# Kernel tuning notes

Measured on AMD Instinct MI355X. Metric: run time of the kernel, lower is better.

## Reference

```python
import jax, jax.numpy as jnp
import numpy as np

DECAY = 0.8
EPS = 1e-05


def setup_inputs() -> dict:
    key = jax.random.key(0)
    k1, k2, k3 = jax.random.split(key, 3)
    B, N, D, H, K = 8, 2048, 64, 1, 8192
    x = jax.random.normal(k1, (B, N, D), dtype=jnp.float32)
    embeddings = jax.random.normal(k2, (H, K, D), dtype=jnp.float32)
    cluster_size = jnp.ones((H, K), dtype=jnp.float32)
    embed_avg = jax.random.normal(k3, (H, K, D), dtype=jnp.float32)
    return {"x": x, "embeddings": embeddings,
            "cluster_size": cluster_size, "embed_avg": embed_avg}


def reference(x, embeddings, cluster_size, embed_avg):
    # x: [B, N, D]; ndim < 4 -> prepend codebook dim h=1, pack to [h, B*N, D]
    B, N, D = x.shape
    H, K, _ = embeddings.shape
    flatten = x.reshape(1, B * N, D)  # h = 1

    # dist = -cdist(flatten, embeddings); argmax(-d) == argmin(d2)
    # squared Euclidean distance via expansion (avoid sqrt; monotone for argmin)
    f2 = jnp.sum(flatten * flatten, axis=-1, keepdims=True)        # [h, n, 1]
    e2 = jnp.sum(embeddings * embeddings, axis=-1)[:, None, :]     # [h, 1, K]
    cross = jnp.einsum('hnd,hkd->hnk', flatten, embeddings)        # [h, n, K]
    d2 = f2 - 2.0 * cross + e2                                     # [h, n, K]
    embed_ind = jnp.argmin(d2, axis=-1)                            # [h, n] int

    # quantize: gather selected codes (== onehot @ embeddings)
    quantize = jnp.take(embeddings[0], embed_ind[0], axis=0).reshape(B, N, D)

    # EMA codebook update (training path) via segment sums (== onehot einsum)
    idx = embed_ind[0]                                             # [B*N]
    cs = jax.ops.segment_sum(jnp.ones_like(idx, dtype=flatten.dtype),
                             idx, num_segments=K)[None, :]         # [h, K]
    embed_sum = jax.ops.segment_sum(flatten[0], idx,
                                    num_segments=K)[None]          # [h, K, D]

    new_cluster_size = cluster_size * DECAY + cs * (1.0 - DECAY)
    new_embed_avg = embed_avg * DECAY + embed_sum * (1.0 - DECAY)

    # laplace smoothing then normalize embed_avg
    total = jnp.sum(new_cluster_size, axis=-1, keepdims=True)      # [h, 1]
    smoothed = (new_cluster_size + EPS) / (total + K * EPS) * total
    embed_normalized = new_embed_avg / smoothed[..., None]         # [h, K, D]

    return quantize, embed_ind.reshape(B, N), embed_normalized, new_cluster_size, new_embed_avg
```

## Files before the change

kernel.cpp:

```cpp
#include <hip/hip_runtime.h>

#define D 64
#define BM 128
#define NCHUNK 8
#define NLIST (2 * NCHUNK)
#define DECAYF 0.8f
#define OMDF 0.2f
#define EPSF 1e-5f
#define INVS 4.8828125e-4f

typedef _Float16 f16;
typedef _Float16 f16x8 __attribute__((ext_vector_type(8)));
typedef float f32x4 __attribute__((ext_vector_type(4)));

__global__ __launch_bounds__(512) void prep_kernel(
    const float* __restrict__ emb, const float* __restrict__ cluster_size,
    f16* __restrict__ eh2, f16* __restrict__ el2, float* __restrict__ e2,
    float* __restrict__ cs_sum, float* __restrict__ ncs, float* __restrict__ nea,
    int K)
{
    __shared__ float red[512];
    int t = blockIdx.x * 512 + threadIdx.x;
    int lane = t & 63;
    int sub  = (t >> 6) & 7;
    int tile = t >> 9;
    int wn = sub >> 2, nf = (sub >> 1) & 1, ks = sub & 1;
    int lrow = lane & 15, lkg = lane >> 4;
    int k  = tile * 64 + wn * 32 + nf * 16 + lrow;
    int d0 = ks * 32 + lkg * 8;

    {
        float4 z = {0.f, 0.f, 0.f, 0.f};
        float4* nea4 = reinterpret_cast<float4*>(nea);
        nea4[t]         = z;
        nea4[t + 65536] = z;
        if (t < 2048) reinterpret_cast<float4*>(ncs)[t] = z;
    }

    const float4* p = reinterpret_cast<const float4*>(emb + (size_t)k * D + d0);
    float4 a = p[0], b = p[1];
    float v[8] = {a.x, a.y, a.z, a.w, b.x, b.y, b.z, b.w};
    union { f16 h[8]; uint4 u; } H, L;
    float part = 0.f;
#pragma unroll
    for (int j = 0; j < 8; ++j) {
        part = fmaf(v[j], v[j], part);
        f16 h = (f16)v[j];
        H.h[j] = h;
        L.h[j] = (f16)((v[j] - (float)h) * 2048.0f);
    }
    reinterpret_cast<uint4*>(eh2)[t] = H.u;
    reinterpret_cast<uint4*>(el2)[t] = L.u;

    red[threadIdx.x] = part;

    if (blockIdx.x < (K >> 9)) {
        float cv = cluster_size[t];
#pragma unroll
        for (int m = 1; m < 64; m <<= 1) cv += __shfl_xor(cv, m, 64);
        if ((threadIdx.x & 63) == 0) atomicAdd(cs_sum, cv);
    }
    __syncthreads();

    if (threadIdx.x < 64) {
        int r = threadIdx.x;
        int rwn = r >> 5, rnf = (r >> 4) & 1, rlr = r & 15;
        float s = 0.f;
#pragma unroll
        for (int kks = 0; kks < 2; ++kks)
#pragma unroll
            for (int g = 0; g < 4; ++g)
                s += red[((rwn * 2 + rnf) * 2 + kks) * 64 + g * 16 + rlr];
        e2[tile * 64 + r] = s;
    }
}

__global__ __launch_bounds__(256, 2) void argmin_kernel(
    const float* __restrict__ x, const f16* __restrict__ eh2, const f16* __restrict__ el2,
    const float* __restrict__ e2, int* __restrict__ pidx, int n, int K)
{
    __shared__ float se2a[1024];

    const int tx   = threadIdx.x;
    const int lane = tx & 63;
    const int wid  = tx >> 6;
    const int wm   = wid >> 1, wn = wid & 1;
    const int lrow = lane & 15;
    const int lkg  = lane >> 4;

    const int chunk = blockIdx.x % NCHUNK;
    const int mblk  = blockIdx.x / NCHUNK;
    const int q0    = mblk * BM;
    const int kc    = K / NCHUNK;
    const int k0    = chunk * kc;
    const int gt0   = chunk * (kc / 64);
    const int NT    = kc / 64;

    f16x8 ah[4][2], al[4][2];
    f32x4 hf2[4];
#pragma unroll
    for (int m = 0; m < 4; ++m) {
        float f2part = 0.f;
#pragma unroll
        for (int ks = 0; ks < 2; ++ks) {
            int row = q0 + wm * 64 + m * 16 + lrow;
            const float4* p = reinterpret_cast<const float4*>(
                x + (size_t)row * D + ks * 32 + lkg * 8);
            float4 va = p[0], vb = p[1];
            float t[8] = {va.x, va.y, va.z, va.w, vb.x, vb.y, vb.z, vb.w};
#pragma unroll
            for (int j = 0; j < 8; ++j) {
                f2part = fmaf(t[j], t[j], f2part);
                float nt = -t[j];
                f16 h = (f16)nt;
                ah[m][ks][j] = h;
                al[m][ks][j] = (f16)((nt - (float)h) * 2048.0f);
            }
        }
        f2part += __shfl_xor(f2part, 16, 64);
        f2part += __shfl_xor(f2part, 32, 64);
#pragma unroll
        for (int r = 0; r < 4; ++r)
            hf2[m][r] = 0.5f * __shfl(f2part, lkg * 4 + r, 64);
    }

    for (int i = tx; i < kc; i += 256) se2a[i] = 0.5f * e2[k0 + i];
    __syncthreads();

    unsigned int pbest[16];
#pragma unroll
    for (int s = 0; s < 16; ++s) pbest[s] = 0xFFFFFFFFu;

    auto LOADB = [&](f16x8 (&BH)[2][2], f16x8 (&BL)[2][2], int ttv) {
        const f16* bhb = eh2 + ((size_t)(gt0 + ttv) << 12);
        const f16* blb = el2 + ((size_t)(gt0 + ttv) << 12);
#pragma unroll
        for (int nf = 0; nf < 2; ++nf)
#pragma unroll
            for (int ks = 0; ks < 2; ++ks) {
                int sub = (wn * 2 + nf) * 2 + ks;
                BH[nf][ks] = *reinterpret_cast<const f16x8*>(bhb + sub * 512 + lane * 8);
                BL[nf][ks] = *reinterpret_cast<const f16x8*>(blb + sub * 512 + lane * 8);
            }
    };

    auto COMPUTE = [&](const f16x8 (&BH)[2][2], const f16x8 (&BL)[2][2], int ttv) {
        const float he0 = se2a[ttv * 64 + wn * 32 + lrow];
        const float he1 = se2a[ttv * 64 + wn * 32 + 16 + lrow];
        const unsigned int tagA = (unsigned int)(ttv * 2);
        const unsigned int tagB = tagA + 1u;
#pragma unroll
        for (int m = 0; m < 4; ++m) {
            f32x4 hh0 = hf2[m] + he0;
            f32x4 hh1 = hf2[m] + he1;
            f32x4 md0 = {0.f, 0.f, 0.f, 0.f};
            f32x4 md1 = {0.f, 0.f, 0.f, 0.f};
            __builtin_amdgcn_s_setprio(1);
            hh0 = __builtin_amdgcn_mfma_f32_16x16x32_f16(ah[m][0], BH[0][0], hh0, 0, 0, 0);
            hh1 = __builtin_amdgcn_mfma_f32_16x16x32_f16(ah[m][0], BH[1][0], hh1, 0, 0, 0);
            hh0 = __builtin_amdgcn_mfma_f32_16x16x32_f16(ah[m][1], BH[0][1], hh0, 0, 0, 0);
            hh1 = __builtin_amdgcn_mfma_f32_16x16x32_f16(ah[m][1], BH[1][1], hh1, 0, 0, 0);
            md0 = __builtin_amdgcn_mfma_f32_16x16x32_f16(al[m][0], BH[0][0], md0, 0, 0, 0);
            md1 = __builtin_amdgcn_mfma_f32_16x16x32_f16(al[m][0], BH[1][0], md1, 0, 0, 0);
            md0 = __builtin_amdgcn_mfma_f32_16x16x32_f16(al[m][1], BH[0][1], md0, 0, 0, 0);
            md1 = __builtin_amdgcn_mfma_f32_16x16x32_f16(al[m][1], BH[1][1], md1, 0, 0, 0);
            md0 = __builtin_amdgcn_mfma_f32_16x16x32_f16(ah[m][0], BL[0][0], md0, 0, 0, 0);
            md1 = __builtin_amdgcn_mfma_f32_16x16x32_f16(ah[m][0], BL[1][0], md1, 0, 0, 0);
            md0 = __builtin_amdgcn_mfma_f32_16x16x32_f16(ah[m][1], BL[0][1], md0, 0, 0, 0);
            md1 = __builtin_amdgcn_mfma_f32_16x16x32_f16(ah[m][1], BL[1][1], md1, 0, 0, 0);
            __builtin_amdgcn_s_setprio(0);
#pragma unroll
            for (int r = 0; r < 4; ++r) {
                float tA = fmaf(md0[r], INVS, hh0[r]);
                float tB = fmaf(md1[r], INVS, hh1[r]);
                unsigned int uA = (__float_as_uint(tA) & 0xFFFFFFE0u) | tagA;
                unsigned int uB = (__float_as_uint(tB) & 0xFFFFFFE0u) | tagB;
                unsigned int w = uA < uB ? uA : uB;
                int s = m * 4 + r;
                pbest[s] = pbest[s] < w ? pbest[s] : w;
            }
        }
    };

    f16x8 bh[2][2], bl[2][2], nh[2][2], nl[2][2];
    LOADB(bh, bl, 0);
#pragma unroll 1
    for (int tt = 0; tt < NT; tt += 2) {
        LOADB(nh, nl, tt + 1);
        COMPUTE(bh, bl, tt);
        if (tt + 2 < NT) LOADB(bh, bl, tt + 2);
        COMPUTE(nh, nl, tt + 1);
    }

#pragma unroll
    for (int s = 0; s < 16; ++s) {
        unsigned int u = pbest[s];
        unsigned int tag = u & 31u;
        int cid = (int)((tag >> 1) << 6) | (int)((tag & 1u) << 4) | (wn << 5) | lrow;
#pragma unroll
        for (int xm = 1; xm < 16; xm <<= 1) {
            unsigned int ou = __shfl_xor(u, xm, 64);
            int          oc = __shfl_xor(cid, xm, 64);
            if (ou < u || (ou == u && oc < cid)) { u = ou; cid = oc; }
        }
        if (lrow == 0) {
            int m = s >> 2, r = s & 3;
            int row = q0 + wm * 64 + m * 16 + lkg * 4 + r;
            pidx[(size_t)(chunk * 2 + wn) * n + row] = k0 + cid;
        }
    }
}

__global__ __launch_bounds__(256) void rerank_kernel(
    const float* __restrict__ x, const float* __restrict__ emb, const float* __restrict__ e2,
    const int* __restrict__ pidx, float* __restrict__ out_ind, float* __restrict__ quant,
    float* __restrict__ embed_sum, float* __restrict__ counts, int n)
{
    int gid  = blockIdx.x * blockDim.x + threadIdx.x;
    int q    = gid >> 6;
    int lane = gid & 63;
    int c    = lane >> 2;
    int j    = lane & 3;
    if (q >= n) return;

    int k = pidx[(size_t)c * n + q];
    const float4* ep = reinterpret_cast<const float4*>(emb + (size_t)k * D);
    const float4* xp = reinterpret_cast<const float4*>(x + (size_t)q * D);

    float a0 = 0.f, a1 = 0.f, a2 = 0.f, a3 = 0.f;
#pragma unroll
    for (int i = 0; i < 4; ++i) {
        float4 e4 = ep[j + 4 * i];
        float4 x4 = xp[j + 4 * i];
        a0 = fmaf(x4.x, e4.x, a0);
        a1 = fmaf(x4.y, e4.y, a1);
        a2 = fmaf(x4.z, e4.z, a2);
        a3 = fmaf(x4.w, e4.w, a3);
    }
    float p = (a0 + a1) + (a2 + a3);
    p += __shfl_xor(p, 1, 64);
    p += __shfl_xor(p, 2, 64);
    float dist = fmaf(p, -2.0f, e2[k]);
    int   bk   = k;

#pragma unroll
    for (int xm = 4; xm < 64; xm <<= 1) {
        float od = __shfl_xor(dist, xm, 64);
        int   ok = __shfl_xor(bk, xm, 64);
        if (od < dist || (od == dist && ok < bk)) { dist = od; bk = ok; }
    }

    float xv = x[(size_t)q * D + lane];
    quant[(size_t)q * D + lane] = emb[(size_t)bk * D + lane];
    atomicAdd(embed_sum + (size_t)bk * D + lane, xv);
    if (lane == 0) {
        out_ind[q] = (float)bk;
        atomicAdd(counts + bk, 1.0f);
    }
}

__global__ __launch_bounds__(256) void ema_kernel(
    const float* __restrict__ cluster_size, const float* __restrict__ embed_avg,
    const float* __restrict__ cs_sum, float* __restrict__ ncs,
    float* __restrict__ nea, float* __restrict__ enorm, int K, int n)
{
    int gid = blockIdx.x * blockDim.x + threadIdx.x;
    if (gid >= K * D) return;
    int k = gid >> 6;
    float total = DECAYF * cs_sum[0] + OMDF * (float)n;
    float cnew  = cluster_size[k] * DECAYF + ncs[k] * OMDF;
    if ((gid & 63) == 0) ncs[k] = cnew;
    float v = embed_avg[gid] * DECAYF + nea[gid] * OMDF;
    nea[gid] = v;
    float smoothed = (cnew + EPSF) / (total + (float)K * EPSF) * total;
    enorm[gid] = v / smoothed;
}

extern "C" void kernel_launch(void* const* d_in, const int* in_sizes, int n_in,
                              void* d_out, int out_size, void* d_ws, size_t ws_size,
                              hipStream_t stream) {
    const float* x            = (const float*)d_in[0];
    const float* emb          = (const float*)d_in[1];
    const float* cluster_size = (const float*)d_in[2];
    const float* embed_avg    = (const float*)d_in[3];

    const int n = in_sizes[0] / D;
    const int K = in_sizes[1] / D;

    float* out     = (float*)d_out;
    float* quant   = out;
    float* out_ind = quant + (size_t)n * D;
    float* enorm   = out_ind + n;
    float* ncs     = enorm + (size_t)K * D;
    float* nea     = ncs + K;

    f16* eh2 = reinterpret_cast<f16*>(enorm);
    f16* el2 = eh2 + (size_t)K * D;

    float* e2     = (float*)d_ws;
    int*   pidx   = (int*)(e2 + K);
    float* cs_sum = (float*)(pidx + (size_t)NLIST * n);

    hipMemsetAsync(cs_sum, 0, sizeof(float), stream);

    prep_kernel<<<K * 8 / 512, 512, 0, stream>>>(
        emb, cluster_size, eh2, el2, e2, cs_sum, ncs, nea, K);
    argmin_kernel<<<(n / BM) * NCHUNK, 256, 0, stream>>>(x, eh2, el2, e2, pidx, n, K);
    rerank_kernel<<<(n * 64 + 255) / 256, 256, 0, stream>>>(
        x, emb, e2, pidx, out_ind, quant, nea, ncs, n);
    ema_kernel<<<(K * D + 255) / 256, 256, 0, stream>>>(
        cluster_size, embed_avg, cs_sum, ncs, nea, enorm, K, n);
}
```

Before: 88.87 us.

## Drop split-fp16 correction MFMAs; keep top-2 candidates per list and rerank more

The argmin pass now uses a single fp16 product instead of the hi/lo split that needed three times the MFMAs and a second codebook copy. To make up for the lost precision, each wave keeps the two best candidates per row instead of one. That doubles the candidate lists, and the exact fp32 rerank kernel then checks 32 candidates per query with 2 lanes each. This cuts matrix-core work and codebook loads, at the cost of more compare logic, more candidate writes and a risk of a wrong argmin when the true best falls outside the fp16 top-2.

Result: slower. 99.14 us (+11.6%).

```diff
diff --git a/kernel.cpp b/kernel.cpp
--- a/kernel.cpp
+++ b/kernel.cpp
@@ -3,11 +3,10 @@
 #define D 64
 #define BM 128
 #define NCHUNK 8
-#define NLIST (2 * NCHUNK)
+#define NLIST (4 * NCHUNK)
 #define DECAYF 0.8f
 #define OMDF 0.2f
 #define EPSF 1e-5f
-#define INVS 4.8828125e-4f
 
 typedef _Float16 f16;
 typedef _Float16 f16x8 __attribute__((ext_vector_type(8)));
@@ -15,7 +14,7 @@
 
 __global__ __launch_bounds__(512) void prep_kernel(
     const float* __restrict__ emb, const float* __restrict__ cluster_size,
-    f16* __restrict__ eh2, f16* __restrict__ el2, float* __restrict__ e2,
+    f16* __restrict__ eh2, float* __restrict__ e2,
     float* __restrict__ cs_sum, float* __restrict__ ncs, float* __restrict__ nea,
     int K)
 {
@@ -40,17 +39,14 @@
     const float4* p = reinterpret_cast<const float4*>(emb + (size_t)k * D + d0);
     float4 a = p[0], b = p[1];
     float v[8] = {a.x, a.y, a.z, a.w, b.x, b.y, b.z, b.w};
-    union { f16 h[8]; uint4 u; } H, L;
+    union { f16 h[8]; uint4 u; } H;
     float part = 0.f;
 #pragma unroll
     for (int j = 0; j < 8; ++j) {
         part = fmaf(v[j], v[j], part);
-        f16 h = (f16)v[j];
-        H.h[j] = h;
-        L.h[j] = (f16)((v[j] - (float)h) * 2048.0f);
+        H.h[j] = (f16)v[j];
     }
     reinterpret_cast<uint4*>(eh2)[t] = H.u;
-    reinterpret_cast<uint4*>(el2)[t] = L.u;
 
     red[threadIdx.x] = part;
 
@@ -76,7 +72,7 @@
 }
 
 __global__ __launch_bounds__(256, 2) void argmin_kernel(
-    const float* __restrict__ x, const f16* __restrict__ eh2, const f16* __restrict__ el2,
+    const float* __restrict__ x, const f16* __restrict__ eh2,
     const float* __restrict__ e2, int* __restrict__ pidx, int n, int K)
 {
     __shared__ float se2a[1024];
@@ -96,7 +92,7 @@
     const int gt0   = chunk * (kc / 64);
     const int NT    = kc / 64;
 
-    f16x8 ah[4][2], al[4][2];
+    f16x8 ah[4][2];
     f32x4 hf2[4];
 #pragma unroll
     for (int m = 0; m < 4; ++m) {
@@ -111,10 +107,7 @@
 #pragma unroll
             for (int j = 0; j < 8; ++j) {
                 f2part = fmaf(t[j], t[j], f2part);
-                float nt = -t[j];
-                f16 h = (f16)nt;
-                ah[m][ks][j] = h;
-                al[m][ks][j] = (f16)((nt - (float)h) * 2048.0f);
+                ah[m][ks][j] = (f16)(-t[j]);
             }
         }
         f2part += __shfl_xor(f2part, 16, 64);
@@ -127,24 +120,22 @@
     for (int i = tx; i < kc; i += 256) se2a[i] = 0.5f * e2[k0 + i];
     __syncthreads();
 
-    unsigned int pbest[16];
-#pragma unroll
-    for (int s = 0; s < 16; ++s) pbest[s] = 0xFFFFFFFFu;
-
-    auto LOADB = [&](f16x8 (&BH)[2][2], f16x8 (&BL)[2][2], int ttv) {
+    unsigned int p1[16], p2[16];
+#pragma unroll
+    for (int s = 0; s < 16; ++s) { p1[s] = 0xFFFFFFFFu; p2[s] = 0xFFFFFFFFu; }
+
+    auto LOADB = [&](f16x8 (&BH)[2][2], int ttv) {
         const f16* bhb = eh2 + ((size_t)(gt0 + ttv) << 12);
-        const f16* blb = el2 + ((size_t)(gt0 + ttv) << 12);
 #pragma unroll
         for (int nf = 0; nf < 2; ++nf)
 #pragma unroll
             for (int ks = 0; ks < 2; ++ks) {
                 int sub = (wn * 2 + nf) * 2 + ks;
                 BH[nf][ks] = *reinterpret_cast<const f16x8*>(bhb + sub * 512 + lane * 8);
-                BL[nf][ks] = *reinterpret_cast<const f16x8*>(blb + sub * 512 + lane * 8);
             }
     };
 
-    auto COMPUTE = [&](const f16x8 (&BH)[2][2], const f16x8 (&BL)[2][2], int ttv) {
+    auto COMPUTE = [&](const f16x8 (&BH)[2][2], int ttv) {
         const float he0 = se2a[ttv * 64 + wn * 32 + lrow];
         const float he1 = se2a[ttv * 64 + wn * 32 + 16 + lrow];
         const unsigned int tagA = (unsigned int)(ttv * 2);
@@ -153,60 +144,65 @@
         for (int m = 0; m < 4; ++m) {
             f32x4 hh0 = hf2[m] + he0;
             f32x4 hh1 = hf2[m] + he1;
-            f32x4 md0 = {0.f, 0.f, 0.f, 0.f};
-            f32x4 md1 = {0.f, 0.f, 0.f, 0.f};
             __builtin_amdgcn_s_setprio(1);
             hh0 = __builtin_amdgcn_mfma_f32_16x16x32_f16(ah[m][0], BH[0][0], hh0, 0, 0, 0);
             hh1 = __builtin_amdgcn_mfma_f32_16x16x32_f16(ah[m][0], BH[1][0], hh1, 0, 0, 0);
             hh0 = __builtin_amdgcn_mfma_f32_16x16x32_f16(ah[m][1], BH[0][1], hh0, 0, 0, 0);
             hh1 = __builtin_amdgcn_mfma_f32_16x16x32_f16(ah[m][1], BH[1][1], hh1, 0, 0, 0);
-            md0 = __builtin_amdgcn_mfma_f32_16x16x32_f16(al[m][0], BH[0][0], md0, 0, 0, 0);
-            md1 = __builtin_amdgcn_mfma_f32_16x16x32_f16(al[m][0], BH[1][0], md1, 0, 0, 0);
-            md0 = __builtin_amdgcn_mfma_f32_16x16x32_f16(al[m][1], BH[0][1], md0, 0, 0, 0);
-            md1 = __builtin_amdgcn_mfma_f32_16x16x32_f16(al[m][1], BH[1][1], md1, 0, 0, 0);
-            md0 = __builtin_amdgcn_mfma_f32_16x16x32_f16(ah[m][0], BL[0][0], md0, 0, 0, 0);
-            md1 = __builtin_amdgcn_mfma_f32_16x16x32_f16(ah[m][0], BL[1][0], md1, 0, 0, 0);
-            md0 = __builtin_amdgcn_mfma_f32_16x16x32_f16(ah[m][1], BL[0][1], md0, 0, 0, 0);
-            md1 = __builtin_amdgcn_mfma_f32_16x16x32_f16(ah[m][1], BL[1][1], md1, 0, 0, 0);
             __builtin_amdgcn_s_setprio(0);
 #pragma unroll
             for (int r = 0; r < 4; ++r) {
-                float tA = fmaf(md0[r], INVS, hh0[r]);
-                float tB = fmaf(md1[r], INVS, hh1[r]);
-                unsigned int uA = (__float_as_uint(tA) & 0xFFFFFFE0u) | tagA;
-                unsigned int uB = (__float_as_uint(tB) & 0xFFFFFFE0u) | tagB;
-                unsigned int w = uA < uB ? uA : uB;
+                unsigned int uA = (__float_as_uint(hh0[r]) & 0xFFFFFFE0u) | tagA;
+                unsigned int uB = (__float_as_uint(hh1[r]) & 0xFFFFFFE0u) | tagB;
+                unsigned int lo = uA < uB ? uA : uB;
+                unsigned int hi = uA < uB ? uB : uA;
                 int s = m * 4 + r;
-                pbest[s] = pbest[s] < w ? pbest[s] : w;
+                unsigned int t1 = p1[s], t2 = p2[s];
+                unsigned int mx = t1 > lo ? t1 : lo;
+                unsigned int mn2 = t2 < hi ? t2 : hi;
+                p1[s] = t1 < lo ? t1 : lo;
+                p2[s] = mx < mn2 ? mx : mn2;
             }
         }
     };
 
-    f16x8 bh[2][2], bl[2][2], nh[2][2], nl[2][2];
-    LOADB(bh, bl, 0);
+    f16x8 bh[2][2], nh[2][2];
+    LOADB(bh, 0);
 #pragma unroll 1
     for (int tt = 0; tt < NT; tt += 2) {
-        LOADB(nh, nl, tt + 1);
-        COMPUTE(bh, bl, tt);
-        if (tt + 2 < NT) LOADB(bh, bl, tt + 2);
-        COMPUTE(nh, nl, tt + 1);
+        LOADB(nh, tt + 1);
+        COMPUTE(bh, tt);
+        if (tt + 2 < NT) LOADB(bh, tt + 2);
+        COMPUTE(nh, tt + 1);
     }
 
 #pragma unroll
     for (int s = 0; s < 16; ++s) {
-        unsigned int u = pbest[s];
-        unsigned int tag = u & 31u;
-        int cid = (int)((tag >> 1) << 6) | (int)((tag & 1u) << 4) | (wn << 5) | lrow;
+        unsigned int u1 = p1[s], u2 = p2[s];
+        unsigned int tg1 = u1 & 31u, tg2 = u2 & 31u;
+        int c1 = (int)((tg1 >> 1) << 6) | (int)((tg1 & 1u) << 4) | (wn << 5) | lrow;
+        int c2 = (int)((tg2 >> 1) << 6) | (int)((tg2 & 1u) << 4) | (wn << 5) | lrow;
 #pragma unroll
         for (int xm = 1; xm < 16; xm <<= 1) {
-            unsigned int ou = __shfl_xor(u, xm, 64);
-            int          oc = __shfl_xor(cid, xm, 64);
-            if (ou < u || (ou == u && oc < cid)) { u = ou; cid = oc; }
+            unsigned int o1 = __shfl_xor(u1, xm, 64);
+            unsigned int o2 = __shfl_xor(u2, xm, 64);
+            int oc1 = __shfl_xor(c1, xm, 64);
+            int oc2 = __shfl_xor(c2, xm, 64);
+            bool a = o1 < u1 || (o1 == u1 && oc1 < c1);
+            unsigned int w1 = a ? o1 : u1;  int wc1 = a ? oc1 : c1;
+            unsigned int l1 = a ? u1 : o1;  int lc1 = a ? c1 : oc1;
+            bool b = o2 < u2 || (o2 == u2 && oc2 < c2);
+            unsigned int m2 = b ? o2 : u2;  int mc2 = b ? oc2 : c2;
+            bool cgt = m2 < l1 || (m2 == l1 && mc2 < lc1);
+            u1 = w1; c1 = wc1;
+            u2 = cgt ? m2 : l1; c2 = cgt ? mc2 : lc1;
         }
         if (lrow == 0) {
             int m = s >> 2, r = s & 3;
             int row = q0 + wm * 64 + m * 16 + lkg * 4 + r;
-            pidx[(size_t)(chunk * 2 + wn) * n + row] = k0 + cid;
+            int list = chunk * 4 + wn * 2;
+            pidx[(size_t)list       * n + row] = k0 + c1;
+            pidx[(size_t)(list + 1) * n + row] = k0 + c2;
         }
     }
 }
@@ -219,8 +215,8 @@
     int gid  = blockIdx.x * blockDim.x + threadIdx.x;
     int q    = gid >> 6;
     int lane = gid & 63;
-    int c    = lane >> 2;
-    int j    = lane & 3;
+    int c    = lane >> 1;
+    int j    = lane & 1;
     if (q >= n) return;
 
     int k = pidx[(size_t)c * n + q];
@@ -229,9 +225,9 @@
 
     float a0 = 0.f, a1 = 0.f, a2 = 0.f, a3 = 0.f;
 #pragma unroll
-    for (int i = 0; i < 4; ++i) {
-        float4 e4 = ep[j + 4 * i];
-        float4 x4 = xp[j + 4 * i];
+    for (int i = 0; i < 8; ++i) {
+        float4 e4 = ep[j * 8 + i];
+        float4 x4 = xp[j * 8 + i];
         a0 = fmaf(x4.x, e4.x, a0);
         a1 = fmaf(x4.y, e4.y, a1);
         a2 = fmaf(x4.z, e4.z, a2);
@@ -239,12 +235,11 @@
     }
     float p = (a0 + a1) + (a2 + a3);
     p += __shfl_xor(p, 1, 64);
-    p += __shfl_xor(p, 2, 64);
     float dist = fmaf(p, -2.0f, e2[k]);
     int   bk   = k;
 
 #pragma unroll
-    for (int xm = 4; xm < 64; xm <<= 1) {
+    for (int xm = 2; xm < 64; xm <<= 1) {
         float od = __shfl_xor(dist, xm, 64);
         int   ok = __shfl_xor(bk, xm, 64);
         if (od < dist || (od == dist && ok < bk)) { dist = od; bk = ok; }
@@ -295,7 +290,6 @@
     float* nea     = ncs + K;
 
     f16* eh2 = reinterpret_cast<f16*>(enorm);
-    f16* el2 = eh2 + (size_t)K * D;
 
     float* e2     = (float*)d_ws;
     int*   pidx   = (int*)(e2 + K);
@@ -304,8 +298,8 @@
     hipMemsetAsync(cs_sum, 0, sizeof(float), stream);
 
     prep_kernel<<<K * 8 / 512, 512, 0, stream>>>(
-        emb, cluster_size, eh2, el2, e2, cs_sum, ncs, nea, K);
-    argmin_kernel<<<(n / BM) * NCHUNK, 256, 0, stream>>>(x, eh2, el2, e2, pidx, n, K);
+        emb, cluster_size, eh2, e2, cs_sum, ncs, nea, K);
+    argmin_kernel<<<(n / BM) * NCHUNK, 256, 0, stream>>>(x, eh2, e2, pidx, n, K);
     rerank_kernel<<<(n * 64 + 255) / 256, 256, 0, stream>>>(
         x, emb, e2, pidx, out_ind, quant, nea, ncs, n);
     ema_kernel<<<(K * D + 255) / 256, 256, 0, stream>>>(
```
